# Performance work log

Measured on AMD Instinct MI355X. Metric: run time of the kernel, lower is better.

## Reference

```python
import jax, jax.numpy as jnp
import numpy as np

N_NODES = 50000
N_EDGES = 1600000
HID = 128
N_LAYERS = 4
EPS = 1e-5
NEG_SLOPE = 0.2


def setup_inputs() -> dict:
    key = jax.random.key(0)
    ks = jax.random.split(key, 10)
    x = jax.random.normal(ks[0], (N_NODES, HID), dtype=jnp.float32)
    edge_index = jax.random.randint(ks[1], (2, N_EDGES), 0, N_NODES, dtype=jnp.int64)
    edge_label_index = jax.random.randint(ks[2], (2, 8192), 0, N_NODES, dtype=jnp.int64)
    s = 1.0 / np.sqrt(HID)
    Wl = jax.random.uniform(ks[3], (N_LAYERS, HID, HID), jnp.float32, -s, s)
    Wr = jax.random.uniform(ks[4], (N_LAYERS, HID, HID), jnp.float32, -s, s)
    att = jax.random.uniform(ks[5], (N_LAYERS, HID), jnp.float32, -s, s)
    bias = jnp.zeros((N_LAYERS, HID), jnp.float32)
    gamma = jnp.ones((N_LAYERS, HID), jnp.float32)
    beta = jnp.zeros((N_LAYERS, HID), jnp.float32)
    return {"x": x, "edge_index": edge_index, "edge_label_index": edge_label_index,
            "Wl": Wl, "Wr": Wr, "att": att, "bias": bias, "gamma": gamma, "beta": beta}


def _gatv2_layer(x, Wl, Wr, a, b, src, dst):
    # GATv2Conv, single head: e_ij = a^T LeakyReLU(W_l x_j + W_r x_i)
    xl = x @ Wl                       # [N, H] source transform (also the message)
    xr = x @ Wr                       # [N, H] target transform
    e = jax.nn.leaky_relu(xl[src] + xr[dst], NEG_SLOPE) @ a   # [E]
    emax = jax.ops.segment_max(e, dst, num_segments=N_NODES)  # per-target max
    ew = jnp.exp(e - emax[dst])
    denom = jax.ops.segment_sum(ew, dst, num_segments=N_NODES)
    alpha = ew / denom[dst]
    out = jax.ops.segment_sum(alpha[:, None] * xl[src], dst, num_segments=N_NODES)
    return out + b


def _batchnorm(x, g, b):
    mu = jnp.mean(x, axis=0)
    var = jnp.mean(jnp.square(x - mu), axis=0)  # biased var (training mode)
    return (x - mu) * jax.lax.rsqrt(var + EPS) * g + b


def _embedding(x, edge_index, Wl, Wr, att, bias, gamma, beta):
    loops = jnp.arange(N_NODES, dtype=edge_index.dtype)
    src = jnp.concatenate([edge_index[0], loops])
    dst = jnp.concatenate([edge_index[1], loops])
    resw = 1.0 / (N_LAYERS + 1)  # alpha buffer, all entries equal
    h = x
    out = None
    for i in range(N_LAYERS):
        h = _gatv2_layer(h, Wl[i], Wr[i], att[i], bias[i], src, dst)
        h = _batchnorm(h, gamma[i], beta[i])
        out = h * resw if out is None else out + h * resw
    return out


def reference(x, edge_index, edge_label_index, Wl, Wr, att, bias, gamma, beta):
    out = _embedding(x, edge_index, Wl, Wr, att, bias, gamma, beta)
    return (out[edge_label_index[0]] * out[edge_label_index[1]]).sum(axis=-1)
```

## Files before the change

kernel.cpp:

```cpp
#include <hip/hip_runtime.h>
#include <hip/hip_bf16.h>
#include <hip/hip_fp16.h>

#define N_NODES 50000
#define N_EDGES 1600000
#define ET (N_EDGES + N_NODES)
#define HID 128
#define N_LAYERS 4
#define EPS 1e-5f
#define NEG 0.2f
#define RB 256
#define NBUCK 782
#define BCHUNK 8192
#define LOG2E 1.44269504088896f

typedef __attribute__((ext_vector_type(8))) short s16x8;
typedef __attribute__((ext_vector_type(8))) __bf16 bfx8;
typedef __attribute__((ext_vector_type(4))) float fx4;
typedef __attribute__((ext_vector_type(2))) _Float16 f16x2;

__device__ __forceinline__ unsigned int packbf2(float a, float b) {
    unsigned int ua = __float_as_uint(a);
    ua = (ua + 0x7fffu + ((ua >> 16) & 1u)) >> 16;
    unsigned int ub = __float_as_uint(b);
    ub = (ub + 0x7fffu + ((ub >> 16) & 1u)) & 0xffff0000u;
    return (ua & 0xffffu) | ub;
}
__device__ __forceinline__ unsigned short bf16r(float a) {
    unsigned int ua = __float_as_uint(a);
    return (unsigned short)((ua + 0x7fffu + ((ua >> 16) & 1u)) >> 16);
}
__device__ __forceinline__ unsigned int packh2(float a, float b) {
    return __builtin_bit_cast(unsigned int, __builtin_amdgcn_cvt_pkrtz(a, b));
}
__device__ __forceinline__ f16x2 packh2v(float a, float b) {
    return __builtin_bit_cast(f16x2, __builtin_amdgcn_cvt_pkrtz(a, b));
}
__device__ __forceinline__ float2 unpackh2(unsigned int u) {
    f16x2 h = __builtin_bit_cast(f16x2, u);
    return make_float2((float)h.x, (float)h.y);
}

__global__ void bucket_zero_kernel(int* __restrict__ gcnt) {
    int i = blockIdx.x * 256 + threadIdx.x;
    if (i < NBUCK) gcnt[i] = 0;
}

__global__ __launch_bounds__(256) void bucket_hist_kernel(const int* __restrict__ ei,
                                                          int* __restrict__ gcnt) {
    __shared__ int h[NBUCK];
    for (int i = threadIdx.x; i < NBUCK; i += 256) h[i] = 0;
    __syncthreads();
    int base = blockIdx.x * BCHUNK;
    int lim = min(base + BCHUNK, ET);
    for (int i = base + threadIdx.x; i < lim; i += 256) {
        int dst = (i < N_EDGES) ? ei[N_EDGES + i] : i - N_EDGES;
        atomicAdd(&h[dst >> 6], 1);
    }
    __syncthreads();
    for (int i = threadIdx.x; i < NBUCK; i += 256)
        if (h[i]) atomicAdd(&gcnt[i], h[i]);
}

__global__ void bucket_scan_kernel(const int* __restrict__ gcnt, int* __restrict__ bbase,
                                   int* __restrict__ bcur, int* __restrict__ rowptr) {
    __shared__ int sh[1024];
    int tid = threadIdx.x;
    int v = (tid < NBUCK) ? gcnt[tid] : 0;
    sh[tid] = v;
    __syncthreads();
    for (int off = 1; off < 1024; off <<= 1) {
        int t = (tid >= off) ? sh[tid - off] : 0;
        __syncthreads();
        sh[tid] += t;
        __syncthreads();
    }
    if (tid < NBUCK) {
        int ex = sh[tid] - v;
        bbase[tid] = ex;
        bcur[tid] = ex;
    }
    if (tid == NBUCK - 1) bbase[NBUCK] = sh[tid];
    if (tid == 0) rowptr[N_NODES] = ET;
}

__global__ __launch_bounds__(256) void bucket_scatter_kernel(const int* __restrict__ ei,
                                                             int* __restrict__ bcur,
                                                             unsigned int* __restrict__ pairs) {
    __shared__ int h[NBUCK];
    __shared__ int rbase[NBUCK];
    for (int i = threadIdx.x; i < NBUCK; i += 256) h[i] = 0;
    __syncthreads();
    int base = blockIdx.x * BCHUNK;
    int lim = min(base + BCHUNK, ET);
    for (int i = base + threadIdx.x; i < lim; i += 256) {
        int dst = (i < N_EDGES) ? ei[N_EDGES + i] : i - N_EDGES;
        atomicAdd(&h[dst >> 6], 1);
    }
    __syncthreads();
    for (int i = threadIdx.x; i < NBUCK; i += 256) {
        rbase[i] = h[i] ? atomicAdd(&bcur[i], h[i]) : 0;
        h[i] = 0;
    }
    __syncthreads();
    for (int i = base + threadIdx.x; i < lim; i += 256) {
        int src, dst;
        if (i < N_EDGES) { src = ei[i]; dst = ei[N_EDGES + i]; }
        else { src = dst = i - N_EDGES; }
        int b = dst >> 6;
        int pos = rbase[b] + atomicAdd(&h[b], 1);
        pairs[pos] = (unsigned int)src | ((unsigned int)(dst & 63) << 16);
    }
}

__global__ __launch_bounds__(256) void bucket_sort_kernel(const unsigned int* __restrict__ pairs,
                                                          const int* __restrict__ bbase,
                                                          int* __restrict__ rowptr,
                                                          unsigned short* __restrict__ csr_src) {
    __shared__ int h[64], ex[64], cur[64];
    int b = blockIdx.x;
    int tid = threadIdx.x;
    if (tid < 64) h[tid] = 0;
    __syncthreads();
    int bs = bbase[b], be = bbase[b + 1];
    for (int i = bs + tid; i < be; i += 256) atomicAdd(&h[pairs[i] >> 16], 1);
    __syncthreads();
    if (tid == 0) {
        int run = 0;
        for (int k = 0; k < 64; k++) { ex[k] = run; cur[k] = run; run += h[k]; }
    }
    __syncthreads();
    int n0 = b * 64;
    if (tid < 64 && n0 + tid < N_NODES) rowptr[n0 + tid] = bs + ex[tid];
    for (int i = bs + tid; i < be; i += 256) {
        unsigned int u = pairs[i];
        int ln = u >> 16;
        int pos = bs + atomicAdd(&cur[ln], 1);
        csr_src[pos] = (unsigned short)(u & 0xffffu);
    }
}

__global__ __launch_bounds__(256) void wconv_kernel(const float* __restrict__ Wl,
                                                    const float* __restrict__ Wr,
                                                    unsigned short* __restrict__ wt) {
    int m = blockIdx.x;
    const float* __restrict__ W = ((m & 1) ? Wr : Wl) + (size_t)(m >> 1) * HID * HID;
    unsigned short* __restrict__ o = wt + (size_t)m * HID * HID;
    for (int i = threadIdx.x; i < HID * HID; i += 256) {
        int k = i >> 7, c = i & 127;
        o[c * HID + k] = bf16r(W[i]);
    }
}

__global__ __launch_bounds__(256) void gemm_mfma_kernel(
    const float* __restrict__ hin_f, const unsigned int* __restrict__ hin_h,
    const unsigned short* __restrict__ wt_layer,
    unsigned int* __restrict__ xlh, unsigned int* __restrict__ xrh,
    const float* __restrict__ scale, const float* __restrict__ shift,
    unsigned int* __restrict__ accb, int donorm, int accmode) {
    __shared__ unsigned int Ash[128 * 64];
    __shared__ unsigned int Wsh[128 * 64];
    int row0 = blockIdx.x * 128;
    int tid = threadIdx.x;
    for (int i = tid; i < 2048; i += 256) {
        int r = i >> 4, ch = i & 15;
        int gr = row0 + r;
        uint4 pk = make_uint4(0u, 0u, 0u, 0u);
        if (gr < N_NODES) {
            float4 va, vb;
            if (hin_h) {
                uint4 u = ((const uint4*)(hin_h + (size_t)gr * 64))[ch];
                float2 f0 = unpackh2(u.x), f1 = unpackh2(u.y);
                float2 f2 = unpackh2(u.z), f3 = unpackh2(u.w);
                va = make_float4(f0.x, f0.y, f1.x, f1.y);
                vb = make_float4(f2.x, f2.y, f3.x, f3.y);
            } else {
                const float4* src = (const float4*)(hin_f + (size_t)gr * HID + ch * 8);
                va = src[0]; vb = src[1];
            }
            if (donorm) {
                const float4* s4 = (const float4*)(scale + ch * 8);
                const float4* t4 = (const float4*)(shift + ch * 8);
                float4 s0 = s4[0], s1 = s4[1], t0 = t4[0], t1 = t4[1];
                va.x = va.x * s0.x + t0.x; va.y = va.y * s0.y + t0.y;
                va.z = va.z * s0.z + t0.z; va.w = va.w * s0.w + t0.w;
                vb.x = vb.x * s1.x + t1.x; vb.y = vb.y * s1.y + t1.y;
                vb.z = vb.z * s1.z + t1.z; vb.w = vb.w * s1.w + t1.w;
            }
            if (accmode && blockIdx.y == 0) {
                uint4* ap = (uint4*)(accb + (size_t)gr * 64) + ch;
                uint4 av;
                if (accmode == 1) {
                    av.x = packh2(0.2f * va.x, 0.2f * va.y);
                    av.y = packh2(0.2f * va.z, 0.2f * va.w);
                    av.z = packh2(0.2f * vb.x, 0.2f * vb.y);
                    av.w = packh2(0.2f * vb.z, 0.2f * vb.w);
                } else {
                    uint4 old = *ap;
                    float2 o0 = unpackh2(old.x), o1 = unpackh2(old.y);
                    float2 o2 = unpackh2(old.z), o3 = unpackh2(old.w);
                    av.x = packh2(o0.x + 0.2f * va.x, o0.y + 0.2f * va.y);
                    av.y = packh2(o1.x + 0.2f * va.z, o1.y + 0.2f * va.w);
                    av.z = packh2(o2.x + 0.2f * vb.x, o2.y + 0.2f * vb.y);
                    av.w = packh2(o3.x + 0.2f * vb.z, o3.y + 0.2f * vb.w);
                }
                *ap = av;
            }
            pk.x = packbf2(va.x, va.y); pk.y = packbf2(va.z, va.w);
            pk.z = packbf2(vb.x, vb.y); pk.w = packbf2(vb.z, vb.w);
        }
        *(uint4*)(&Ash[r * 64 + ((ch ^ (r & 7)) << 2)]) = pk;
    }
    {
        const uint4* wm4 = (const uint4*)(wt_layer + (size_t)blockIdx.y * HID * HID);
        for (int i = tid; i < 2048; i += 256) {
            int c = i >> 4, ch = i & 15;
            uint4 v = wm4[i];
            *(uint4*)(&Wsh[c * 64 + ((ch ^ (c & 7)) << 2)]) = v;
        }
    }
    __syncthreads();

    int l = tid & 63, w = tid >> 6;
    int lr = l & 15, lk = l >> 4;
    fx4 acc0[8], acc1[8];
#pragma unroll
    for (int ct = 0; ct < 8; ct++) {
        acc0[ct] = (fx4){0.f, 0.f, 0.f, 0.f};
        acc1[ct] = (fx4){0.f, 0.f, 0.f, 0.f};
    }
#pragma unroll
    for (int kt = 0; kt < 4; kt++) {
        int ch = kt * 4 + lk;
        int n0 = w * 32 + lr, n1 = n0 + 16;
        bfx8 b0 = __builtin_bit_cast(bfx8, *(const s16x8*)(&Ash[n0 * 64 + ((ch ^ (n0 & 7)) << 2)]));
        bfx8 b1 = __builtin_bit_cast(bfx8, *(const s16x8*)(&Ash[n1 * 64 + ((ch ^ (n1 & 7)) << 2)]));
#pragma unroll
        for (int ct = 0; ct < 8; ct++) {
            int c = ct * 16 + lr;
            bfx8 aw = __builtin_bit_cast(bfx8, *(const s16x8*)(&Wsh[c * 64 + ((ch ^ (c & 7)) << 2)]));
            acc0[ct] = __builtin_amdgcn_mfma_f32_16x16x32_bf16(aw, b0, acc0[ct], 0, 0, 0);
            acc1[ct] = __builtin_amdgcn_mfma_f32_16x16x32_bf16(aw, b1, acc1[ct], 0, 0, 0);
        }
    }
    unsigned int* o = blockIdx.y ? xrh : xlh;
    int g0 = row0 + w * 32 + lr, g1 = g0 + 16;
#pragma unroll
    for (int ct = 0; ct < 8; ct++) {
        int cb = ct * 8 + lk * 2;
        if (g0 < N_NODES) {
            uint2 p0;
            p0.x = packh2(acc0[ct][0], acc0[ct][1]);
            p0.y = packh2(acc0[ct][2], acc0[ct][3]);
            *(uint2*)(o + (size_t)g0 * 64 + cb) = p0;
        }
        if (g1 < N_NODES) {
            uint2 p1;
            p1.x = packh2(acc1[ct][0], acc1[ct][1]);
            p1.y = packh2(acc1[ct][2], acc1[ct][3]);
            *(uint2*)(o + (size_t)g1 * 64 + cb) = p1;
        }
    }
}

__global__ __launch_bounds__(256) void aggregate_kernel(
    const unsigned int* __restrict__ xlh, const unsigned int* __restrict__ xrh,
    const float* __restrict__ att, const float* __restrict__ bias,
    const int* __restrict__ rowptr, const unsigned short* __restrict__ csr_src,
    unsigned int* __restrict__ hout) {
    int node = blockIdx.x * 16 + (threadIdx.x >> 4);
    if (node >= N_NODES) return;
    int g = threadIdx.x & 15;
    int c0 = g * 8;
    float4 aa = *(const float4*)(att + c0);
    float4 ab = *(const float4*)(att + c0 + 4);
    f16x2 a0 = packh2v(aa.x * LOG2E, aa.y * LOG2E);
    f16x2 a1 = packh2v(aa.z * LOG2E, aa.w * LOG2E);
    f16x2 a2 = packh2v(ab.x * LOG2E, ab.y * LOG2E);
    f16x2 a3 = packh2v(ab.z * LOG2E, ab.w * LOG2E);
    const uint4 ru = *(const uint4*)(xrh + (size_t)node * 64 + g * 4);
    f16x2 r0 = __builtin_bit_cast(f16x2, ru.x), r1 = __builtin_bit_cast(f16x2, ru.y);
    f16x2 r2 = __builtin_bit_cast(f16x2, ru.z), r3 = __builtin_bit_cast(f16x2, ru.w);
    const f16x2 negc = {(_Float16)NEG, (_Float16)NEG};
    int beg = rowptr[node], end = rowptr[node + 1];
    bool b0 = (g & 1) != 0, b1 = (g & 2) != 0, b2 = (g & 4) != 0;
    int myj = g & 7;
    float spart = 0.f;
    float acc0 = 0.f, acc1 = 0.f, acc2 = 0.f, acc3 = 0.f;
    float acc4 = 0.f, acc5 = 0.f, acc6 = 0.f, acc7 = 0.f;
    int idxc = (int)csr_src[min(beg + myj, end - 1)];
    for (int base = beg; base < end; base += 8) {
        int nn = end - base;
        if (nn > 8) nn = 8;
        int idxn = (base + 8 < end) ? (int)csr_src[min(base + 8 + myj, end - 1)] : 0;
        uint4 v[8];
#pragma unroll
        for (int j = 0; j < 8; j++) {
            int sj = __shfl(idxc, j, 8);
            v[j] = *(const uint4*)(xlh + (size_t)sj * 64 + g * 4);
        }
        float p[8];
#pragma unroll
        for (int j = 0; j < 8; j++) {
            f16x2 v0 = __builtin_bit_cast(f16x2, v[j].x);
            f16x2 v1 = __builtin_bit_cast(f16x2, v[j].y);
            f16x2 v2 = __builtin_bit_cast(f16x2, v[j].z);
            f16x2 v3 = __builtin_bit_cast(f16x2, v[j].w);
            f16x2 s0 = v0 + r0, s1 = v1 + r1, s2 = v2 + r2, s3 = v3 + r3;
            f16x2 m0 = __builtin_elementwise_max(s0, s0 * negc);
            f16x2 m1 = __builtin_elementwise_max(s1, s1 * negc);
            f16x2 m2 = __builtin_elementwise_max(s2, s2 * negc);
            f16x2 m3 = __builtin_elementwise_max(s3, s3 * negc);
            p[j] = __builtin_amdgcn_fdot2(m0, a0,
                     __builtin_amdgcn_fdot2(m1, a1,
                       __builtin_amdgcn_fdot2(m2, a2,
                         __builtin_amdgcn_fdot2(m3, a3, 0.f, false), false), false), false);
        }
        float q0 = (b0 ? p[1] : p[0]) + __shfl_xor(b0 ? p[0] : p[1], 1);
        float q1 = (b0 ? p[3] : p[2]) + __shfl_xor(b0 ? p[2] : p[3], 1);
        float q2 = (b0 ? p[5] : p[4]) + __shfl_xor(b0 ? p[4] : p[5], 1);
        float q3 = (b0 ? p[7] : p[6]) + __shfl_xor(b0 ? p[6] : p[7], 1);
        float t0 = (b1 ? q1 : q0) + __shfl_xor(b1 ? q0 : q1, 2);
        float t1 = (b1 ? q3 : q2) + __shfl_xor(b1 ? q2 : q3, 2);
        float f  = (b2 ? t1 : t0) + __shfl_xor(b2 ? t0 : t1, 4);
        f += __shfl_xor(f, 8);
        float wown = (myj < nn) ? exp2f(f) : 0.f;
        spart += wown;
#pragma unroll
        for (int j = 0; j < 8; j++) {
            float wj = __shfl(wown, j, 8);
            f16x2 v0 = __builtin_bit_cast(f16x2, v[j].x);
            f16x2 v1 = __builtin_bit_cast(f16x2, v[j].y);
            f16x2 v2 = __builtin_bit_cast(f16x2, v[j].z);
            f16x2 v3 = __builtin_bit_cast(f16x2, v[j].w);
            acc0 += wj * (float)v0.x; acc1 += wj * (float)v0.y;
            acc2 += wj * (float)v1.x; acc3 += wj * (float)v1.y;
            acc4 += wj * (float)v2.x; acc5 += wj * (float)v2.y;
            acc6 += wj * (float)v3.x; acc7 += wj * (float)v3.y;
        }
        idxc = idxn;
    }
    float s = spart;
    s += __shfl_xor(s, 1);
    s += __shfl_xor(s, 2);
    s += __shfl_xor(s, 4);
    float inv = 1.f / s;
    float4 ba = *(const float4*)(bias + c0);
    float4 bb = *(const float4*)(bias + c0 + 4);
    uint4 po;
    po.x = packh2(acc0 * inv + ba.x, acc1 * inv + ba.y);
    po.y = packh2(acc2 * inv + ba.z, acc3 * inv + ba.w);
    po.z = packh2(acc4 * inv + bb.x, acc5 * inv + bb.y);
    po.w = packh2(acc6 * inv + bb.z, acc7 * inv + bb.w);
    *(uint4*)(hout + (size_t)node * 64 + g * 4) = po;
}

__global__ __launch_bounds__(256) void bn_reduce_kernel(const unsigned int* __restrict__ h,
                                                        float* __restrict__ part) {
    int tid = threadIdx.x;
    int cu = tid & 63, half = tid >> 6;
    float s0 = 0.f, q0 = 0.f, s1 = 0.f, q1 = 0.f;
    for (int r = blockIdx.x * 4 + half; r < N_NODES; r += RB * 4) {
        float2 v = unpackh2(h[(size_t)r * 64 + cu]);
        s0 += v.x; q0 += v.x * v.x;
        s1 += v.y; q1 += v.y * v.y;
    }
    __shared__ float sh[256];
    sh[half * 64 + cu] = s0;
    __syncthreads();
    if (tid < 64) {
        float r0 = sh[tid] + sh[64 + tid] + sh[128 + tid] + sh[192 + tid];
        part[blockIdx.x * 256 + tid * 2] = r0;
    }
    __syncthreads();
    sh[half * 64 + cu] = q0;
    __syncthreads();
    if (tid < 64) {
        float r0 = sh[tid] + sh[64 + tid] + sh[128 + tid] + sh[192 + tid];
        part[blockIdx.x * 256 + 128 + tid * 2] = r0;
    }
    __syncthreads();
    sh[half * 64 + cu] = s1;
    __syncthreads();
    if (tid < 64) {
        float r0 = sh[tid] + sh[64 + tid] + sh[128 + tid] + sh[192 + tid];
        part[blockIdx.x * 256 + tid * 2 + 1] = r0;
    }
    __syncthreads();
    sh[half * 64 + cu] = q1;
    __syncthreads();
    if (tid < 64) {
        float r0 = sh[tid] + sh[64 + tid] + sh[128 + tid] + sh[192 + tid];
        part[blockIdx.x * 256 + 128 + tid * 2 + 1] = r0;
    }
}

__global__ void bn_finalize_kernel(const float* __restrict__ part,
                                   const float* __restrict__ gamma,
                                   const float* __restrict__ beta,
                                   float* __restrict__ scale, float* __restrict__ shift) {
    int c = threadIdx.x;
    float s = 0.f, q = 0.f;
    for (int b = 0; b < RB; b++) {
        s += part[b * 256 + c];
        q += part[b * 256 + 128 + c];
    }
    float m = s / (float)N_NODES;
    float v = q / (float)N_NODES - m * m;
    if (v < 0.f) v = 0.f;
    float rs = rsqrtf(v + EPS);
    float sc = rs * gamma[c];
    scale[c] = sc;
    shift[c] = beta[c] - m * sc;
}

__global__ __launch_bounds__(256) void accb_kernel(const unsigned int* __restrict__ h,
                                                   const float* __restrict__ scale,
                                                   const float* __restrict__ shift,
                                                   unsigned int* __restrict__ acc) {
    int idx = blockIdx.x * 256 + threadIdx.x;
    if (idx >= N_NODES * 64) return;
    int c = (idx & 63) * 2;
    float2 v = unpackh2(h[idx]);
    float n0 = v.x * scale[c] + shift[c];
    float n1 = v.y * scale[c + 1] + shift[c + 1];
    float2 a = unpackh2(acc[idx]);
    acc[idx] = packh2(a.x + 0.2f * n0, a.y + 0.2f * n1);
}

__global__ __launch_bounds__(256) void predict_kernel(const unsigned int* __restrict__ acc,
                                                      const int* __restrict__ eli,
                                                      float* __restrict__ out) {
    int p = blockIdx.x * 4 + (threadIdx.x >> 6);
    if (p >= 8192) return;
    int lane = threadIdx.x & 63;
    int i = eli[p], j = eli[8192 + p];
    f16x2 va = __builtin_bit_cast(f16x2, acc[(size_t)i * 64 + lane]);
    f16x2 vb = __builtin_bit_cast(f16x2, acc[(size_t)j * 64 + lane]);
    float t = (float)va.x * (float)vb.x + (float)va.y * (float)vb.y;
#pragma unroll
    for (int off = 32; off; off >>= 1) t += __shfl_xor(t, off, 64);
    if (lane == 0) out[p] = t;
}

extern "C" void kernel_launch(void* const* d_in, const int* in_sizes, int n_in,
                              void* d_out, int out_size, void* d_ws, size_t ws_size,
                              hipStream_t stream) {
    const float* x = (const float*)d_in[0];
    const int* ei = (const int*)d_in[1];
    const int* eli = (const int*)d_in[2];
    const float* Wl = (const float*)d_in[3];
    const float* Wr = (const float*)d_in[4];
    const float* att = (const float*)d_in[5];
    const float* bias = (const float*)d_in[6];
    const float* gamma = (const float*)d_in[7];
    const float* beta = (const float*)d_in[8];
    float* out = (float*)d_out;

    char* ws = (char*)d_ws;
    size_t off = 0;
    unsigned int* hbuf = (unsigned int*)(ws + off); off += (size_t)N_NODES * HID * 2;
    unsigned int* accb = (unsigned int*)(ws + off); off += (size_t)N_NODES * HID * 2;
    unsigned int* xlh  = (unsigned int*)(ws + off); off += (size_t)N_NODES * HID * 2;
    unsigned int* xrh  = (unsigned int*)(ws + off); off += (size_t)N_NODES * HID * 2;
    int* rowptr = (int*)(ws + off);   off += ((size_t)(N_NODES + 1) * 4 + 31) & ~31ul;
    unsigned short* csr_src = (unsigned short*)(ws + off); off += ((size_t)(ET + 16) * 2 + 31) & ~31ul;
    int* gcnt  = (int*)(ws + off);    off += (size_t)NBUCK * 4;
    int* bcur  = (int*)(ws + off);    off += (size_t)NBUCK * 4;
    int* bbase = (int*)(ws + off);    off += (size_t)(NBUCK + 1) * 4;
    float* part = (float*)(ws + off); off += (size_t)RB * 256 * 4;
    float* scale = (float*)(ws + off); off += 128 * 4;
    float* shift = (float*)(ws + off); off += 128 * 4;
    unsigned short* wt = (unsigned short*)(ws + off); off += (size_t)8 * HID * HID * 2;
    unsigned int* pairs = (unsigned int*)(ws + off); off += (size_t)ET * 4;

    wconv_kernel<<<8, 256, 0, stream>>>(Wl, Wr, wt);

    int nablk = (ET + BCHUNK - 1) / BCHUNK;
    bucket_zero_kernel<<<(NBUCK + 255) / 256, 256, 0, stream>>>(gcnt);
    bucket_hist_kernel<<<nablk, 256, 0, stream>>>(ei, gcnt);
    bucket_scan_kernel<<<1, 1024, 0, stream>>>(gcnt, bbase, bcur, rowptr);
    bucket_scatter_kernel<<<nablk, 256, 0, stream>>>(ei, bcur, pairs);
    bucket_sort_kernel<<<NBUCK, 256, 0, stream>>>(pairs, bbase, rowptr, csr_src);

    for (int l = 0; l < N_LAYERS; l++) {
        int donorm = (l == 0) ? 0 : 1;
        int accmode = (l == 0) ? 0 : (l == 1 ? 1 : 2);
        gemm_mfma_kernel<<<dim3((N_NODES + 127) / 128, 2), 256, 0, stream>>>(
            (l == 0) ? x : nullptr, (l == 0) ? nullptr : hbuf,
            wt + (size_t)l * 2 * HID * HID, xlh, xrh, scale, shift, accb,
            donorm, accmode);
        aggregate_kernel<<<(N_NODES + 15) / 16, 256, 0, stream>>>(
            xlh, xrh, att + l * HID, bias + l * HID, rowptr, csr_src, hbuf);
        bn_reduce_kernel<<<RB, 256, 0, stream>>>(hbuf, part);
        bn_finalize_kernel<<<1, 128, 0, stream>>>(part, gamma + l * HID, beta + l * HID,
                                                  scale, shift);
    }
    accb_kernel<<<(N_NODES * 64 + 255) / 256, 256, 0, stream>>>(hbuf, scale, shift, accb);
    predict_kernel<<<8192 / 4, 256, 0, stream>>>(accb, eli, out);
}
```

Measured before the change: 504.7 us.

## Sort nodes by degree class so aggregate wavefronts get balanced work

Adds a counting sort of nodes by in-degree bucket (histogram, scan, scatter) that builds a permutation, and the aggregate kernel now processes nodes in that order. Nodes handled by the same block or wavefront then have similar edge counts, which reduces divergence and idle lanes in the per-node edge loop. The cost is three extra small kernels per call and scattered node reads and writes in the aggregation, which lose the locality of consecutive node ids.

```diff
diff --git a/kernel.cpp b/kernel.cpp
--- a/kernel.cpp
+++ b/kernel.cpp
@@ -41,9 +41,10 @@
     return make_float2((float)h.x, (float)h.y);
 }
 
-__global__ void bucket_zero_kernel(int* __restrict__ gcnt) {
+__global__ void bucket_zero_kernel(int* __restrict__ gcnt, int* __restrict__ dhist) {
     int i = blockIdx.x * 256 + threadIdx.x;
     if (i < NBUCK) gcnt[i] = 0;
+    if (i < 256) dhist[i] = 0;
 }
 
 __global__ __launch_bounds__(256) void bucket_hist_kernel(const int* __restrict__ ei,
@@ -137,6 +138,39 @@
         int ln = u >> 16;
         int pos = bs + atomicAdd(&cur[ln], 1);
         csr_src[pos] = (unsigned short)(u & 0xffffu);
+    }
+}
+
+__global__ void deg_hist_kernel(const int* __restrict__ rowptr, int* __restrict__ dhist) {
+    int n = blockIdx.x * 256 + threadIdx.x;
+    if (n < N_NODES) {
+        int cc = min((rowptr[n + 1] - rowptr[n] + 7) >> 3, 255);
+        atomicAdd(&dhist[cc], 1);
+    }
+}
+
+__global__ void deg_scan_kernel(const int* __restrict__ dhist, int* __restrict__ dcur) {
+    __shared__ int sh[256];
+    int t = threadIdx.x;
+    int v = dhist[t];
+    sh[t] = v;
+    __syncthreads();
+    for (int off = 1; off < 256; off <<= 1) {
+        int u = (t >= off) ? sh[t - off] : 0;
+        __syncthreads();
+        sh[t] += u;
+        __syncthreads();
+    }
+    dcur[t] = sh[t] - v;
+}
+
+__global__ void deg_scatter_kernel(const int* __restrict__ rowptr, int* __restrict__ dcur,
+                                   int* __restrict__ perm) {
+    int n = blockIdx.x * 256 + threadIdx.x;
+    if (n < N_NODES) {
+        int cc = min((rowptr[n + 1] - rowptr[n] + 7) >> 3, 255);
+        int pos = atomicAdd(&dcur[cc], 1);
+        perm[pos] = n;
     }
 }
 
@@ -267,9 +301,10 @@
     const unsigned int* __restrict__ xlh, const unsigned int* __restrict__ xrh,
     const float* __restrict__ att, const float* __restrict__ bias,
     const int* __restrict__ rowptr, const unsigned short* __restrict__ csr_src,
-    unsigned int* __restrict__ hout) {
-    int node = blockIdx.x * 16 + (threadIdx.x >> 4);
-    if (node >= N_NODES) return;
+    const int* __restrict__ perm, unsigned int* __restrict__ hout) {
+    int slot = blockIdx.x * 16 + (threadIdx.x >> 4);
+    if (slot >= N_NODES) return;
+    int node = perm[slot];
     int g = threadIdx.x & 15;
     int c0 = g * 8;
     float4 aa = *(const float4*)(att + c0);
@@ -468,6 +503,9 @@
     int* gcnt  = (int*)(ws + off);    off += (size_t)NBUCK * 4;
     int* bcur  = (int*)(ws + off);    off += (size_t)NBUCK * 4;
     int* bbase = (int*)(ws + off);    off += (size_t)(NBUCK + 1) * 4;
+    int* dhist = (int*)(ws + off);    off += 256 * 4;
+    int* dcur  = (int*)(ws + off);    off += 256 * 4;
+    int* perm  = (int*)(ws + off);    off += (size_t)N_NODES * 4;
     float* part = (float*)(ws + off); off += (size_t)RB * 256 * 4;
     float* scale = (float*)(ws + off); off += 128 * 4;
     float* shift = (float*)(ws + off); off += 128 * 4;
@@ -477,11 +515,15 @@
     wconv_kernel<<<8, 256, 0, stream>>>(Wl, Wr, wt);
 
     int nablk = (ET + BCHUNK - 1) / BCHUNK;
-    bucket_zero_kernel<<<(NBUCK + 255) / 256, 256, 0, stream>>>(gcnt);
+    bucket_zero_kernel<<<(NBUCK + 255) / 256, 256, 0, stream>>>(gcnt, dhist);
     bucket_hist_kernel<<<nablk, 256, 0, stream>>>(ei, gcnt);
     bucket_scan_kernel<<<1, 1024, 0, stream>>>(gcnt, bbase, bcur, rowptr);
     bucket_scatter_kernel<<<nablk, 256, 0, stream>>>(ei, bcur, pairs);
     bucket_sort_kernel<<<NBUCK, 256, 0, stream>>>(pairs, bbase, rowptr, csr_src);
+
+    deg_hist_kernel<<<(N_NODES + 255) / 256, 256, 0, stream>>>(rowptr, dhist);
+    deg_scan_kernel<<<1, 256, 0, stream>>>(dhist, dcur);
+    deg_scatter_kernel<<<(N_NODES + 255) / 256, 256, 0, stream>>>(rowptr, dcur, perm);
 
     for (int l = 0; l < N_LAYERS; l++) {
         int donorm = (l == 0) ? 0 : 1;
@@ -491,7 +533,7 @@
             wt + (size_t)l * 2 * HID * HID, xlh, xrh, scale, shift, accb,
             donorm, accmode);
         aggregate_kernel<<<(N_NODES + 15) / 16, 256, 0, stream>>>(
-            xlh, xrh, att + l * HID, bias + l * HID, rowptr, csr_src, hbuf);
+            xlh, xrh, att + l * HID, bias + l * HID, rowptr, csr_src, perm, hbuf);
         bn_reduce_kernel<<<RB, 256, 0, stream>>>(hbuf, part);
         bn_finalize_kernel<<<1, 128, 0, stream>>>(part, gamma + l * HID, beta + l * HID,
                                                   scale, shift);
```

Result: slower. 1.178 ms (+133.4%).
